# Performance work log

Measured on AMD Instinct MI355X. Metric: run time of the kernel, lower is better.

Reference implementation:

```python
import jax, jax.numpy as jnp
import numpy as np

N_NODES = 50000
N_EDGES = 800000
IN_DIM = 128
HID = 64
HEADS = 4
OUT_DIM = 20
NUM_GRAPHS = 64
NEG_SLOPE = 0.2  # PyG GATConv default leaky_relu slope


def _xavier(key, shape):
    fan_in, fan_out = shape[-1], shape[0]
    lim = float(np.sqrt(6.0 / (fan_in + fan_out)))
    return jax.random.uniform(key, shape, jnp.float32, -lim, lim)


def setup_inputs() -> dict:
    key = jax.random.key(0)
    ks = jax.random.split(key, 12)
    x = jax.random.normal(ks[0], (N_NODES, IN_DIM), jnp.float32)
    edge_index = jax.random.randint(ks[1], (2, N_EDGES), 0, N_NODES, jnp.int32)
    batch = jnp.sort(jax.random.randint(ks[2], (N_NODES,), 0, NUM_GRAPHS, jnp.int32))
    return {
        "x": x,
        "edge_index": edge_index,
        "batch": batch,
        # conv1: in -> HEADS*HID, concat
        "W1": _xavier(ks[3], (HEADS * HID, IN_DIM)),
        "a_src1": _xavier(ks[4], (HEADS, HID)),
        "a_dst1": _xavier(ks[5], (HEADS, HID)),
        "b1": jnp.zeros((HEADS * HID,), jnp.float32),
        # conv2: HEADS*HID -> HID, 1 head
        "W2": _xavier(ks[6], (HID, HEADS * HID)),
        "a_src2": _xavier(ks[7], (1, HID)),
        "a_dst2": _xavier(ks[8], (1, HID)),
        "b2": jnp.zeros((HID,), jnp.float32),
        "fc_W": _xavier(ks[9], (OUT_DIM, HID)),
        "fc_b": jnp.zeros((OUT_DIM,), jnp.float32),
    }


def _gat_conv(x, src, dst, W, a_src, a_dst, b, heads):
    """PyG GATConv: linear -> per-edge LeakyReLU attention -> softmax over
    incoming edges of each target node -> weighted scatter-sum. Self-loops
    are already included in (src, dst). Dropout omitted (eval mode)."""
    n = x.shape[0]
    h = (x @ W.T).reshape(n, heads, -1)            # [N, H, C]
    alpha_s = jnp.einsum("nhc,hc->nh", h, a_src)   # [N, H]
    alpha_d = jnp.einsum("nhc,hc->nh", h, a_dst)
    e = jax.nn.leaky_relu(alpha_s[src] + alpha_d[dst], NEG_SLOPE)  # [E, H]
    # numerically stable segment softmax over dst
    e_max = jax.ops.segment_max(e, dst, num_segments=n)
    e = jnp.exp(e - e_max[dst])
    denom = jax.ops.segment_sum(e, dst, num_segments=n)
    alpha = e / (denom[dst] + 1e-16)               # [E, H]
    msg = h[src] * alpha[..., None]                # [E, H, C]
    out = jax.ops.segment_sum(msg, dst, num_segments=n)  # [N, H, C]
    return out.reshape(n, -1) + b                  # concat heads


def reference(x, edge_index, batch, W1, a_src1, a_dst1, b1,
              W2, a_src2, a_dst2, b2, fc_W, fc_b):
    n = x.shape[0]
    loops = jnp.arange(n, dtype=edge_index.dtype)
    src = jnp.concatenate([edge_index[0], loops])  # add self-loops (PyG default)
    dst = jnp.concatenate([edge_index[1], loops])
    h = jax.nn.elu(_gat_conv(x, src, dst, W1, a_src1, a_dst1, b1, HEADS))
    h = jax.nn.elu(_gat_conv(h, src, dst, W2, a_src2, a_dst2, b2, 1))
    pooled = jax.ops.segment_max(h, batch, num_segments=NUM_GRAPHS)  # [G, HID]
    return pooled @ fc_W.T + fc_b                  # [G, OUT_DIM]
```

## Files before the change

### kernel.cpp

```cpp
#include <hip/hip_runtime.h>
#include <hip/hip_bf16.h>

#define N_NODES_C 50000
#define N_EDGES_C 800000
#define IN_DIM_C  128
#define HID_C     64
#define HEADS_C   4
#define OUT_DIM_C 20
#define NUM_GRAPHS_C 64
#define NEG_SLOPE 0.2f
#define BUCKET_CAP 64

typedef __attribute__((ext_vector_type(8))) short bf16x8;
typedef __attribute__((ext_vector_type(4))) float f32x4;
typedef __attribute__((ext_vector_type(2))) float f32x2;

__device__ __forceinline__ float lrelu(float t){ return fmaxf(t, NEG_SLOPE*t); }
__device__ __forceinline__ float elu1(float t){ return t > 0.f ? t : __expf(t)-1.f; }
__device__ __forceinline__ ushort f2bf(float f){
  unsigned u = __float_as_uint(f);
  return (ushort)((u + 0x7fffu + ((u>>16)&1u)) >> 16);
}
__device__ __forceinline__ float bflo(unsigned u){ return __uint_as_float(u<<16); }
__device__ __forceinline__ float bfhi(unsigned u){ return __uint_as_float(u & 0xffff0000u); }
__device__ __forceinline__ float bfs(ushort u){ return __uint_as_float(((unsigned)u)<<16); }

__global__ void fillB_kernel(const int* __restrict__ ei, int* __restrict__ cnt,
                             int* __restrict__ adj){
  int e = blockIdx.x*256 + threadIdx.x;
  if (e >= N_EDGES_C) return;
  int sI = ei[e]; int d = ei[N_EDGES_C + e];
  int p = atomicAdd(&cnt[d], 1);
  if (p < BUCKET_CAP) adj[(d<<6) + p] = sI;
}

__global__ __launch_bounds__(256) void wperm_kernel(const float* __restrict__ W1, const float* __restrict__ W2,
    ushort* __restrict__ Wp1h, ushort* __restrict__ Wp1l,
    ushort* __restrict__ Wp2h, ushort* __restrict__ Wp2l){
  int i = blockIdx.x*256 + threadIdx.x;
  const float* src; ushort *dh, *dl; int gidx;
  if(i < 4096){
    int kc = i>>10, oc = (i>>6)&15, l = i&63;
    src = W1 + (size_t)(oc*16 + (l&15))*IN_DIM_C + kc*32 + (l>>4)*8;
    dh = Wp1h; dl = Wp1l; gidx = i;
  } else if(i < 4096+2048){
    int i2 = i - 4096;
    int kc = i2>>8, oc = (i2>>6)&3, l = i2&63;
    src = W2 + (size_t)(oc*16 + (l&15))*256 + kc*32 + (l>>4)*8;
    dh = Wp2h; dl = Wp2l; gidx = i2;
  } else return;
  ushort h8[8], l8[8];
  #pragma unroll
  for(int j=0;j<8;j++){
    float f = src[j];
    ushort h = f2bf(f);
    h8[j] = h; l8[j] = f2bf(f - bfs(h));
  }
  #pragma unroll
  for(int j=0;j<8;j++){ dh[gidx*8+j] = h8[j]; dl[gidx*8+j] = l8[j]; }
}

#define HS1_STRIDE 260
__global__ __launch_bounds__(256) void lin1_mfma(const float* __restrict__ x,
    const ushort* __restrict__ Wp1h, const ushort* __restrict__ Wp1l,
    const float* __restrict__ aS, const float* __restrict__ aD,
    ushort* __restrict__ h1, float* __restrict__ as1, float* __restrict__ ad1){
  __shared__ ushort hs[64*HS1_STRIDE];
  int t = threadIdx.x, w = t>>6, l = t&63;
  int n0b = blockIdx.x*64;
  int n0 = n0b + w*16;
  bool active = (n0 < N_NODES_C);
  int row = l & 15, kg = l >> 4;
  if(active){
    bf16x8 ah[4], al[4];
    int gn = n0 + row; if(gn > N_NODES_C-1) gn = N_NODES_C-1;
    const float* xrow = x + (size_t)gn*IN_DIM_C + kg*8;
    #pragma unroll
    for(int kc=0;kc<4;kc++){
      float4 f0 = *(const float4*)(xrow + kc*32);
      float4 f1 = *(const float4*)(xrow + kc*32 + 4);
      float fv[8] = {f0.x,f0.y,f0.z,f0.w,f1.x,f1.y,f1.z,f1.w};
      #pragma unroll
      for(int j=0;j<8;j++){
        ushort h = f2bf(fv[j]);
        float r = fv[j] - bfs(h);
        ah[kc][j] = (short)h;
        al[kc][j] = (short)f2bf(r);
      }
    }
    const bf16x8* Wh = (const bf16x8*)Wp1h + l;
    const bf16x8* Wl = (const bf16x8*)Wp1l + l;
    f32x4 acc[16];
    #pragma unroll
    for(int oc=0;oc<16;oc++){
      f32x4 a = {0.f,0.f,0.f,0.f};
      const bf16x8* ph = Wh + oc*64;
      const bf16x8* pl = Wl + oc*64;
      #pragma unroll
      for(int kc=0;kc<4;kc++){
        bf16x8 bh = ph[kc*1024];
        bf16x8 bl = pl[kc*1024];
        a = __builtin_amdgcn_mfma_f32_16x16x32_bf16(ah[kc], bh, a, 0, 0, 0);
        a = __builtin_amdgcn_mfma_f32_16x16x32_bf16(ah[kc], bl, a, 0, 0, 0);
        a = __builtin_amdgcn_mfma_f32_16x16x32_bf16(al[kc], bh, a, 0, 0, 0);
      }
      acc[oc] = a;
    }
    #pragma unroll
    for(int h=0;h<4;h++){
      float ps0=0.f,ps1=0.f,ps2=0.f,ps3=0.f, pd0=0.f,pd1=0.f,pd2=0.f,pd3=0.f;
      #pragma unroll
      for(int oi=0;oi<4;oi++){
        int oc = h*4 + oi;
        float as_ = aS[oc*16 + row];
        float ad_ = aD[oc*16 + row];
        ps0 = fmaf(acc[oc][0], as_, ps0); pd0 = fmaf(acc[oc][0], ad_, pd0);
        ps1 = fmaf(acc[oc][1], as_, ps1); pd1 = fmaf(acc[oc][1], ad_, pd1);
        ps2 = fmaf(acc[oc][2], as_, ps2); pd2 = fmaf(acc[oc][2], ad_, pd2);
        ps3 = fmaf(acc[oc][3], as_, ps3); pd3 = fmaf(acc[oc][3], ad_, pd3);
      }
      #pragma unroll
      for(int d=1; d<16; d<<=1){
        ps0 += __shfl_xor(ps0,d); ps1 += __shfl_xor(ps1,d);
        ps2 += __shfl_xor(ps2,d); ps3 += __shfl_xor(ps3,d);
        pd0 += __shfl_xor(pd0,d); pd1 += __shfl_xor(pd1,d);
        pd2 += __shfl_xor(pd2,d); pd3 += __shfl_xor(pd3,d);
      }
      if(row==0){
        int nb4 = (n0 + kg*4)*4 + h;
        as1[nb4+0] = ps0; as1[nb4+4] = ps1; as1[nb4+8] = ps2; as1[nb4+12] = ps3;
        ad1[nb4+0] = pd0; ad1[nb4+4] = pd1; ad1[nb4+8] = pd2; ad1[nb4+12] = pd3;
      }
    }
    #pragma unroll
    for(int oc=0;oc<16;oc++){
      #pragma unroll
      for(int r=0;r<4;r++){
        hs[(w*16 + kg*4 + r)*HS1_STRIDE + oc*16 + row] = f2bf(acc[oc][r]);
      }
    }
  }
  __syncthreads();
  int nvalid = N_NODES_C - n0b; if(nvalid > 64) nvalid = 64;
  for(int i=t; i<nvalid*32; i+=256){
    int r = i>>5, c = i&31;
    ((uint4*)(h1 + (size_t)(n0b+r)*256))[c] = *(const uint4*)(hs + r*HS1_STRIDE + c*8);
  }
}

__global__ __launch_bounds__(256) void agg1_kernel(const int* __restrict__ cnt, const int* __restrict__ adj,
    const ushort* __restrict__ h1,
    const float* __restrict__ as1, const float* __restrict__ ad1,
    const float* __restrict__ b1, float* __restrict__ out1){
  int wv = threadIdx.x>>6, lane = threadIdx.x&63;
  int v = blockIdx.x*4 + wv;
  int head = lane>>4;
  int start = v<<6;
  int end = start + min(cnt[v], BUCKET_CAP);
  float adh = ad1[(v<<2)+head];
  float ash = as1[(v<<2)+head];
  float wself = __expf(lrelu(ash+adh));
  float denom = wself;
  const char* hb = (const char*)h1;
  unsigned loff = ((unsigned)lane)<<3;
  uint2 pv = *(const uint2*)(hb + ((((unsigned)v)<<9) + loff));
  f32x2 acc01 = {wself*bflo(pv.x), wself*bfhi(pv.x)};
  f32x2 acc23 = {wself*bflo(pv.y), wself*bfhi(pv.y)};
  int i = start;
  for(; i+8 <= end; i += 8){
    int s0 = adj[i],   s1 = adj[i+1], s2 = adj[i+2], s3 = adj[i+3];
    int s4 = adj[i+4], s5 = adj[i+5], s6 = adj[i+6], s7 = adj[i+7];
    float a0 = as1[(s0<<2)+head], a1 = as1[(s1<<2)+head];
    float a2 = as1[(s2<<2)+head], a3 = as1[(s3<<2)+head];
    float a4 = as1[(s4<<2)+head], a5 = as1[(s5<<2)+head];
    float a6 = as1[(s6<<2)+head], a7 = as1[(s7<<2)+head];
    uint2 p0 = *(const uint2*)(hb + ((((unsigned)s0)<<9) + loff));
    uint2 p1 = *(const uint2*)(hb + ((((unsigned)s1)<<9) + loff));
    uint2 p2 = *(const uint2*)(hb + ((((unsigned)s2)<<9) + loff));
    uint2 p3 = *(const uint2*)(hb + ((((unsigned)s3)<<9) + loff));
    uint2 p4 = *(const uint2*)(hb + ((((unsigned)s4)<<9) + loff));
    uint2 p5 = *(const uint2*)(hb + ((((unsigned)s5)<<9) + loff));
    uint2 p6 = *(const uint2*)(hb + ((((unsigned)s6)<<9) + loff));
    uint2 p7 = *(const uint2*)(hb + ((((unsigned)s7)<<9) + loff));
    float w0 = __expf(lrelu(a0+adh)), w1 = __expf(lrelu(a1+adh));
    float w2 = __expf(lrelu(a2+adh)), w3 = __expf(lrelu(a3+adh));
    float w4 = __expf(lrelu(a4+adh)), w5 = __expf(lrelu(a5+adh));
    float w6 = __expf(lrelu(a6+adh)), w7 = __expf(lrelu(a7+adh));
    denom += ((w0+w1)+(w2+w3)) + ((w4+w5)+(w6+w7));
    f32x2 W;
    W.x = w0; W.y = w0;
    acc01 = __builtin_elementwise_fma(W, (f32x2){bflo(p0.x), bfhi(p0.x)}, acc01);
    acc23 = __builtin_elementwise_fma(W, (f32x2){bflo(p0.y), bfhi(p0.y)}, acc23);
    W.x = w1; W.y = w1;
    acc01 = __builtin_elementwise_fma(W, (f32x2){bflo(p1.x), bfhi(p1.x)}, acc01);
    acc23 = __builtin_elementwise_fma(W, (f32x2){bflo(p1.y), bfhi(p1.y)}, acc23);
    W.x = w2; W.y = w2;
    acc01 = __builtin_elementwise_fma(W, (f32x2){bflo(p2.x), bfhi(p2.x)}, acc01);
    acc23 = __builtin_elementwise_fma(W, (f32x2){bflo(p2.y), bfhi(p2.y)}, acc23);
    W.x = w3; W.y = w3;
    acc01 = __builtin_elementwise_fma(W, (f32x2){bflo(p3.x), bfhi(p3.x)}, acc01);
    acc23 = __builtin_elementwise_fma(W, (f32x2){bflo(p3.y), bfhi(p3.y)}, acc23);
    W.x = w4; W.y = w4;
    acc01 = __builtin_elementwise_fma(W, (f32x2){bflo(p4.x), bfhi(p4.x)}, acc01);
    acc23 = __builtin_elementwise_fma(W, (f32x2){bflo(p4.y), bfhi(p4.y)}, acc23);
    W.x = w5; W.y = w5;
    acc01 = __builtin_elementwise_fma(W, (f32x2){bflo(p5.x), bfhi(p5.x)}, acc01);
    acc23 = __builtin_elementwise_fma(W, (f32x2){bflo(p5.y), bfhi(p5.y)}, acc23);
    W.x = w6; W.y = w6;
    acc01 = __builtin_elementwise_fma(W, (f32x2){bflo(p6.x), bfhi(p6.x)}, acc01);
    acc23 = __builtin_elementwise_fma(W, (f32x2){bflo(p6.y), bfhi(p6.y)}, acc23);
    W.x = w7; W.y = w7;
    acc01 = __builtin_elementwise_fma(W, (f32x2){bflo(p7.x), bfhi(p7.x)}, acc01);
    acc23 = __builtin_elementwise_fma(W, (f32x2){bflo(p7.y), bfhi(p7.y)}, acc23);
  }
  for(; i < end; i++){
    int s0 = adj[i];
    float a0 = as1[(s0<<2)+head];
    uint2 p0 = *(const uint2*)(hb + ((((unsigned)s0)<<9) + loff));
    float w0 = __expf(lrelu(a0+adh));
    denom += w0;
    f32x2 W; W.x = w0; W.y = w0;
    acc01 = __builtin_elementwise_fma(W, (f32x2){bflo(p0.x), bfhi(p0.x)}, acc01);
    acc23 = __builtin_elementwise_fma(W, (f32x2){bflo(p0.y), bfhi(p0.y)}, acc23);
  }
  float inv = 1.f/(denom + 1e-16f);
  float4 bv = *(const float4*)(b1 + (lane<<2));
  float4 r;
  r.x = elu1(acc01.x*inv + bv.x);
  r.y = elu1(acc01.y*inv + bv.y);
  r.z = elu1(acc23.x*inv + bv.z);
  r.w = elu1(acc23.y*inv + bv.w);
  *(float4*)(out1 + ((size_t)v<<8) + (lane<<2)) = r;
}

#define HS2_STRIDE 68
__global__ __launch_bounds__(256) void lin2_mfma(const float* __restrict__ in,
    const ushort* __restrict__ Wp2h, const ushort* __restrict__ Wp2l,
    const float* __restrict__ aS, const float* __restrict__ aD,
    ushort* __restrict__ h2, float* __restrict__ as2, float* __restrict__ ad2){
  __shared__ ushort hs[64*HS2_STRIDE];
  int t = threadIdx.x, w = t>>6, l = t&63;
  int n0b = blockIdx.x*64;
  int n0 = n0b + w*16;
  bool active = (n0 < N_NODES_C);
  int row = l & 15, kg = l >> 4;
  if(active){
    bf16x8 ah[8], al[8];
    int gn = n0 + row; if(gn > N_NODES_C-1) gn = N_NODES_C-1;
    const float* xrow = in + (size_t)gn*256 + kg*8;
    #pragma unroll
    for(int kc=0;kc<8;kc++){
      float4 f0 = *(const float4*)(xrow + kc*32);
      float4 f1 = *(const float4*)(xrow + kc*32 + 4);
      float fv[8] = {f0.x,f0.y,f0.z,f0.w,f1.x,f1.y,f1.z,f1.w};
      #pragma unroll
      for(int j=0;j<8;j++){
        ushort h = f2bf(fv[j]);
        float r = fv[j] - bfs(h);
        ah[kc][j] = (short)h;
        al[kc][j] = (short)f2bf(r);
      }
    }
    const bf16x8* Wh = (const bf16x8*)Wp2h + l;
    const bf16x8* Wl = (const bf16x8*)Wp2l + l;
    f32x4 acc[4];
    #pragma unroll
    for(int oc=0;oc<4;oc++){
      f32x4 a = {0.f,0.f,0.f,0.f};
      const bf16x8* ph = Wh + oc*64;
      const bf16x8* pl = Wl + oc*64;
      #pragma unroll
      for(int kc=0;kc<8;kc++){
        bf16x8 bh = ph[kc*256];
        bf16x8 bl = pl[kc*256];
        a = __builtin_amdgcn_mfma_f32_16x16x32_bf16(ah[kc], bh, a, 0, 0, 0);
        a = __builtin_amdgcn_mfma_f32_16x16x32_bf16(ah[kc], bl, a, 0, 0, 0);
        a = __builtin_amdgcn_mfma_f32_16x16x32_bf16(al[kc], bh, a, 0, 0, 0);
      }
      acc[oc] = a;
    }
    {
      float ps0=0.f,ps1=0.f,ps2=0.f,ps3=0.f, pd0=0.f,pd1=0.f,pd2=0.f,pd3=0.f;
      #pragma unroll
      for(int oc=0;oc<4;oc++){
        float as_ = aS[oc*16 + row];
        float ad_ = aD[oc*16 + row];
        ps0 = fmaf(acc[oc][0], as_, ps0); pd0 = fmaf(acc[oc][0], ad_, pd0);
        ps1 = fmaf(acc[oc][1], as_, ps1); pd1 = fmaf(acc[oc][1], ad_, pd1);
        ps2 = fmaf(acc[oc][2], as_, ps2); pd2 = fmaf(acc[oc][2], ad_, pd2);
        ps3 = fmaf(acc[oc][3], as_, ps3); pd3 = fmaf(acc[oc][3], ad_, pd3);
      }
      #pragma unroll
      for(int d=1; d<16; d<<=1){
        ps0 += __shfl_xor(ps0,d); ps1 += __shfl_xor(ps1,d);
        ps2 += __shfl_xor(ps2,d); ps3 += __shfl_xor(ps3,d);
        pd0 += __shfl_xor(pd0,d); pd1 += __shfl_xor(pd1,d);
        pd2 += __shfl_xor(pd2,d); pd3 += __shfl_xor(pd3,d);
      }
      if(row==0){
        int n = n0 + kg*4;
        as2[n+0] = ps0; as2[n+1] = ps1; as2[n+2] = ps2; as2[n+3] = ps3;
        ad2[n+0] = pd0; ad2[n+1] = pd1; ad2[n+2] = pd2; ad2[n+3] = pd3;
      }
    }
    #pragma unroll
    for(int oc=0;oc<4;oc++){
      #pragma unroll
      for(int r=0;r<4;r++){
        hs[(w*16 + kg*4 + r)*HS2_STRIDE + oc*16 + row] = f2bf(acc[oc][r]);
      }
    }
  }
  __syncthreads();
  int nvalid = N_NODES_C - n0b; if(nvalid > 64) nvalid = 64;
  for(int i=t; i<nvalid*8; i+=256){
    int r = i>>3, c = i&7;
    ((uint4*)(h2 + (size_t)(n0b+r)*64))[c] = *(const uint4*)(hs + r*HS2_STRIDE + c*8);
  }
}

__global__ __launch_bounds__(256) void agg2_kernel(const int* __restrict__ cnt, const int* __restrict__ adj,
    const ushort* __restrict__ h2,
    const float* __restrict__ as2, const float* __restrict__ ad2,
    const float* __restrict__ b2, float* __restrict__ out2){
  int wv = threadIdx.x>>6, lane = threadIdx.x&63;
  int v = blockIdx.x*4 + wv;
  int half = lane>>5, sl = lane&31;
  int start = v<<6;
  int end = start + min(cnt[v], BUCKET_CAP);
  float adv = ad2[v], asv = as2[v];
  float wself = __expf(lrelu(asv+adv));
  const unsigned* hu = (const unsigned*)h2;
  float denom = half ? 0.f : wself;
  f32x2 acc = {0.f, 0.f};
  if(!half){
    unsigned us = hu[(((unsigned)v)<<5) + sl];
    acc.x = wself*bflo(us); acc.y = wself*bfhi(us);
  }
  int i = start + half;
  for(; i+2 < end; i += 4){
    int sA = adj[i], sB = adj[i+2];
    float aA = as2[sA], aB = as2[sB];
    unsigned uA = hu[(((unsigned)sA)<<5) + sl];
    unsigned uB = hu[(((unsigned)sB)<<5) + sl];
    float wA = __expf(lrelu(aA+adv));
    float wB = __expf(lrelu(aB+adv));
    denom += wA + wB;
    f32x2 W;
    W.x = wA; W.y = wA;
    acc = __builtin_elementwise_fma(W, (f32x2){bflo(uA), bfhi(uA)}, acc);
    W.x = wB; W.y = wB;
    acc = __builtin_elementwise_fma(W, (f32x2){bflo(uB), bfhi(uB)}, acc);
  }
  for(; i < end; i += 2){
    int s = adj[i];
    float wg = __expf(lrelu(as2[s]+adv));
    unsigned u = hu[(((unsigned)s)<<5) + sl];
    denom += wg;
    f32x2 W; W.x = wg; W.y = wg;
    acc = __builtin_elementwise_fma(W, (f32x2){bflo(u), bfhi(u)}, acc);
  }
  acc.x += __shfl_xor(acc.x, 32);
  acc.y += __shfl_xor(acc.y, 32);
  denom += __shfl_xor(denom, 32);
  if(!half){
    float inv = 1.f/(denom + 1e-16f);
    float2 bv = *(const float2*)(b2 + sl*2);
    float2 r;
    r.x = elu1(acc.x*inv + bv.x);
    r.y = elu1(acc.y*inv + bv.y);
    *(float2*)(out2 + (((size_t)v)<<6) + sl*2) = r;
  }
}

__global__ __launch_bounds__(256) void pool_fc_kernel(const float* __restrict__ out2, const int* __restrict__ batch,
    const float* __restrict__ fcW, const float* __restrict__ fcb, float* __restrict__ out){
  int g = blockIdx.x;
  int tid=threadIdx.x; int c = tid&63; int slot = tid>>6;
  int lo=0, hi=N_NODES_C;
  while(lo<hi){ int mid=(lo+hi)>>1; if(batch[mid] < g) lo=mid+1; else hi=mid; }
  int start=lo;
  hi=N_NODES_C;
  while(lo<hi){ int mid=(lo+hi)>>1; if(batch[mid] < g+1) lo=mid+1; else hi=mid; }
  int end=lo;
  float mm = -INFINITY;
  #pragma unroll 4
  for(int n=start+slot; n<end; n+=4) mm = fmaxf(mm, out2[(size_t)n*64+c]);
  __shared__ float sred[4][64];
  sred[slot][c]=mm;
  __syncthreads();
  if(tid < 64){
    float p = fmaxf(fmaxf(sred[0][tid],sred[1][tid]), fmaxf(sred[2][tid],sred[3][tid]));
    sred[0][tid]=p;
  }
  __syncthreads();
  if(tid < OUT_DIM_C){
    float acc = fcb[tid];
    #pragma unroll
    for(int cc=0;cc<64;cc++) acc = fmaf(sred[0][cc], fcW[tid*64+cc], acc);
    out[g*OUT_DIM_C + tid] = acc;
  }
}

extern "C" void kernel_launch(void* const* d_in, const int* in_sizes, int n_in,
                              void* d_out, int out_size, void* d_ws, size_t ws_size,
                              hipStream_t stream) {
  const float* x   = (const float*)d_in[0];
  const int*   ei  = (const int*)  d_in[1];
  const int*   bat = (const int*)  d_in[2];
  const float* W1  = (const float*)d_in[3];
  const float* aS1 = (const float*)d_in[4];
  const float* aD1 = (const float*)d_in[5];
  const float* b1  = (const float*)d_in[6];
  const float* W2  = (const float*)d_in[7];
  const float* aS2 = (const float*)d_in[8];
  const float* aD2 = (const float*)d_in[9];
  const float* b2  = (const float*)d_in[10];
  const float* fcW = (const float*)d_in[11];
  const float* fcb = (const float*)d_in[12];
  float* out = (float*)d_out;

  char* w = (char*)d_ws;
  size_t off = 0;
  auto alloc = [&](size_t bytes)->char* {
    char* p = w + off; off = (off + bytes + 255) & ~(size_t)255; return p;
  };
  int* cnt       = (int*)alloc((size_t)N_NODES_C*sizeof(int));
  int* adj       = (int*)alloc((size_t)N_NODES_C*BUCKET_CAP*sizeof(int));
  ushort* Wp1h   = (ushort*)alloc((size_t)4096*8*sizeof(ushort));
  ushort* Wp1l   = (ushort*)alloc((size_t)4096*8*sizeof(ushort));
  ushort* Wp2h   = (ushort*)alloc((size_t)2048*8*sizeof(ushort));
  ushort* Wp2l   = (ushort*)alloc((size_t)2048*8*sizeof(ushort));
  ushort* h1     = (ushort*)alloc((size_t)N_NODES_C*256*sizeof(ushort));
  float* as1     = (float*)alloc((size_t)N_NODES_C*4*sizeof(float));
  float* ad1     = (float*)alloc((size_t)N_NODES_C*4*sizeof(float));
  float* out1    = (float*)alloc((size_t)N_NODES_C*256*sizeof(float));
  ushort* h2  = h1;
  float* as2  = as1;
  float* ad2  = ad1;
  float* out2 = out1;
  (void)ws_size; (void)in_sizes; (void)n_in; (void)out_size;

  hipMemsetAsync(cnt, 0, (size_t)N_NODES_C*sizeof(int), stream);
  fillB_kernel<<<(N_EDGES_C+255)/256, 256, 0, stream>>>(ei, cnt, adj);
  wperm_kernel<<<24, 256, 0, stream>>>(W1, W2, Wp1h, Wp1l, Wp2h, Wp2l);

  lin1_mfma<<<(N_NODES_C+63)/64, 256, 0, stream>>>(x, Wp1h, Wp1l, aS1, aD1, h1, as1, ad1);
  agg1_kernel<<<N_NODES_C/4, 256, 0, stream>>>(cnt, adj, h1, as1, ad1, b1, out1);
  lin2_mfma<<<(N_NODES_C+63)/64, 256, 0, stream>>>(out1, Wp2h, Wp2l, aS2, aD2, h2, as2, ad2);
  agg2_kernel<<<N_NODES_C/4, 256, 0, stream>>>(cnt, adj, h2, as2, ad2, b2, out2);
  pool_fc_kernel<<<NUM_GRAPHS_C, 256, 0, stream>>>(out2, bat, fcW, fcb, out);
}
```

Measured before the change: 352.2 us.

## Merge edge bucketing with weight permute, pad LDS strides, unroll agg2 loop

Merges the edge-bucketing kernel and the weight split/permute kernel into one launch by giving each a range of block IDs, saving one launch and its gap. Raises the shared-memory row strides in both linear kernels (260 to 264, 68 to 72 ushorts), likely to change bank mapping or alignment of the staged outputs. Unrolls the layer-2 aggregation loop from two to four neighbors per half-wave so more gathers are in flight, at the cost of more registers.

```diff
diff --git a/kernel.cpp b/kernel.cpp
--- a/kernel.cpp
+++ b/kernel.cpp
@@ -10,6 +10,7 @@
 #define NUM_GRAPHS_C 64
 #define NEG_SLOPE 0.2f
 #define BUCKET_CAP 64
+#define FILL_BLOCKS ((N_EDGES_C+255)/256)
 
 typedef __attribute__((ext_vector_type(8))) short bf16x8;
 typedef __attribute__((ext_vector_type(4))) float f32x4;
@@ -25,19 +26,21 @@
 __device__ __forceinline__ float bfhi(unsigned u){ return __uint_as_float(u & 0xffff0000u); }
 __device__ __forceinline__ float bfs(ushort u){ return __uint_as_float(((unsigned)u)<<16); }
 
-__global__ void fillB_kernel(const int* __restrict__ ei, int* __restrict__ cnt,
-                             int* __restrict__ adj){
-  int e = blockIdx.x*256 + threadIdx.x;
-  if (e >= N_EDGES_C) return;
-  int sI = ei[e]; int d = ei[N_EDGES_C + e];
-  int p = atomicAdd(&cnt[d], 1);
-  if (p < BUCKET_CAP) adj[(d<<6) + p] = sI;
-}
-
-__global__ __launch_bounds__(256) void wperm_kernel(const float* __restrict__ W1, const float* __restrict__ W2,
-    ushort* __restrict__ Wp1h, ushort* __restrict__ Wp1l,
-    ushort* __restrict__ Wp2h, ushort* __restrict__ Wp2l){
-  int i = blockIdx.x*256 + threadIdx.x;
+__global__ void fill_wperm_kernel(const int* __restrict__ ei, int* __restrict__ cnt,
+                                  int* __restrict__ adj,
+                                  const float* __restrict__ W1, const float* __restrict__ W2,
+                                  ushort* __restrict__ Wp1h, ushort* __restrict__ Wp1l,
+                                  ushort* __restrict__ Wp2h, ushort* __restrict__ Wp2l){
+  int b = blockIdx.x;
+  if(b < FILL_BLOCKS){
+    int e = b*256 + threadIdx.x;
+    if (e >= N_EDGES_C) return;
+    int sI = ei[e]; int d = ei[N_EDGES_C + e];
+    int p = atomicAdd(&cnt[d], 1);
+    if (p < BUCKET_CAP) adj[(d<<6) + p] = sI;
+    return;
+  }
+  int i = (b - FILL_BLOCKS)*256 + threadIdx.x;
   const float* src; ushort *dh, *dl; int gidx;
   if(i < 4096){
     int kc = i>>10, oc = (i>>6)&15, l = i&63;
@@ -60,7 +63,7 @@
   for(int j=0;j<8;j++){ dh[gidx*8+j] = h8[j]; dl[gidx*8+j] = l8[j]; }
 }
 
-#define HS1_STRIDE 260
+#define HS1_STRIDE 264
 __global__ __launch_bounds__(256) void lin1_mfma(const float* __restrict__ x,
     const ushort* __restrict__ Wp1h, const ushort* __restrict__ Wp1l,
     const float* __restrict__ aS, const float* __restrict__ aD,
@@ -233,7 +236,7 @@
   *(float4*)(out1 + ((size_t)v<<8) + (lane<<2)) = r;
 }
 
-#define HS2_STRIDE 68
+#define HS2_STRIDE 72
 __global__ __launch_bounds__(256) void lin2_mfma(const float* __restrict__ in,
     const ushort* __restrict__ Wp2h, const ushort* __restrict__ Wp2l,
     const float* __restrict__ aS, const float* __restrict__ aD,
@@ -338,19 +341,27 @@
     acc.x = wself*bflo(us); acc.y = wself*bfhi(us);
   }
   int i = start + half;
-  for(; i+2 < end; i += 4){
-    int sA = adj[i], sB = adj[i+2];
-    float aA = as2[sA], aB = as2[sB];
+  for(; i+6 < end; i += 8){
+    int sA = adj[i], sB = adj[i+2], sC = adj[i+4], sD = adj[i+6];
+    float aA = as2[sA], aB = as2[sB], aC = as2[sC], aD_ = as2[sD];
     unsigned uA = hu[(((unsigned)sA)<<5) + sl];
     unsigned uB = hu[(((unsigned)sB)<<5) + sl];
+    unsigned uC = hu[(((unsigned)sC)<<5) + sl];
+    unsigned uD = hu[(((unsigned)sD)<<5) + sl];
     float wA = __expf(lrelu(aA+adv));
     float wB = __expf(lrelu(aB+adv));
-    denom += wA + wB;
+    float wC = __expf(lrelu(aC+adv));
+    float wD = __expf(lrelu(aD_+adv));
+    denom += (wA + wB) + (wC + wD);
     f32x2 W;
     W.x = wA; W.y = wA;
     acc = __builtin_elementwise_fma(W, (f32x2){bflo(uA), bfhi(uA)}, acc);
     W.x = wB; W.y = wB;
     acc = __builtin_elementwise_fma(W, (f32x2){bflo(uB), bfhi(uB)}, acc);
+    W.x = wC; W.y = wC;
+    acc = __builtin_elementwise_fma(W, (f32x2){bflo(uC), bfhi(uC)}, acc);
+    W.x = wD; W.y = wD;
+    acc = __builtin_elementwise_fma(W, (f32x2){bflo(uD), bfhi(uD)}, acc);
   }
   for(; i < end; i += 2){
     int s = adj[i];
@@ -442,8 +453,7 @@
   (void)ws_size; (void)in_sizes; (void)n_in; (void)out_size;
 
   hipMemsetAsync(cnt, 0, (size_t)N_NODES_C*sizeof(int), stream);
-  fillB_kernel<<<(N_EDGES_C+255)/256, 256, 0, stream>>>(ei, cnt, adj);
-  wperm_kernel<<<24, 256, 0, stream>>>(W1, W2, Wp1h, Wp1l, Wp2h, Wp2l);
+  fill_wperm_kernel<<<FILL_BLOCKS + 24, 256, 0, stream>>>(ei, cnt, adj, W1, W2, Wp1h, Wp1l, Wp2h, Wp2l);
 
   lin1_mfma<<<(N_NODES_C+63)/64, 256, 0, stream>>>(x, Wp1h, Wp1l, aS1, aD1, h1, as1, ad1);
   agg1_kernel<<<N_NODES_C/4, 256, 0, stream>>>(cnt, adj, h1, as1, ad1, b1, out1);
```

Result: faster. 344.6 us (-2.2%).
